# Performance work log

Measured on AMD Instinct MI355X. Metric: run time of the kernel, lower is better.

Reference implementation:

```python
import jax, jax.numpy as jnp
import numpy as np

B, T, F, D = 4, 512, 512, 256


def setup_inputs() -> dict:
    key = jax.random.key(0)
    ks = jax.random.split(key, 7)
    x = jax.random.normal(ks[0], (B, T, F), jnp.float32)
    state = jnp.zeros((B, D, D), jnp.float32)
    init = lambda k, shape, fan: jax.random.normal(k, shape, jnp.float32) / np.sqrt(fan).astype(np.float32)
    Wk = init(ks[1], (F, D), F)
    Wq = init(ks[2], (F, D), F)
    Wv = init(ks[3], (F, D), F)
    Wbeta = init(ks[4], (F, 1), F)
    gamma = jnp.ones((F,), jnp.float32)
    beta_ln = jnp.zeros((F,), jnp.float32)
    Wsc = init(ks[5], (F, D), F)
    bsc = jnp.zeros((D,), jnp.float32)
    return dict(x=x, state=state, Wk=Wk, Wq=Wq, Wv=Wv, Wbeta=Wbeta,
                gamma=gamma, beta_ln=beta_ln, Wsc=Wsc, bsc=bsc)


def _layernorm(x, gamma, beta):
    mu = x.mean(-1, keepdims=True)
    var = x.var(-1, keepdims=True)  # ddof=0, matches torch LayerNorm
    return (x - mu) * jax.lax.rsqrt(var + 1e-5) * gamma + beta


def reference(x, state, Wk, Wq, Wv, Wbeta, gamma, beta_ln, Wsc, bsc):
    xn = _layernorm(x, gamma, beta_ln)                       # [B,T,F]
    K = jax.nn.relu(xn @ Wk)                                 # [B,T,D]
    Q = jax.nn.relu(xn @ Wq)                                 # [B,T,D]
    V = xn @ Wv                                              # [B,T,D]
    beta = jax.nn.sigmoid(xn @ Wbeta)                        # [B,T,1]
    # sum normalization
    K = K / (1e-5 + K.sum(-1, keepdims=True))
    Q = Q / (1e-5 + Q.sum(-1, keepdims=True))

    def step(s, inp):
        k, v, b = inp                                        # k,v:[B,D], b:[B,1]
        vbar = jnp.einsum('bij,bj->bi', s, k)                # retrieve
        s = s + (b * (v - vbar))[:, :, None] * k[:, None, :] # outer-product write
        return s, s

    Kt = jnp.moveaxis(K, 1, 0)  # [T,B,D]
    Vt = jnp.moveaxis(V, 1, 0)
    bt = jnp.moveaxis(beta, 1, 0)  # [T,B,1]
    _, states = jax.lax.scan(step, state, (Kt, Vt, bt))      # [T,B,D,D]
    states = jnp.moveaxis(states, 0, 1)                      # [B,T,D,D]

    y = jnp.einsum('btij,btj->bti', states, Q)               # [B,T,D]
    y = y + xn @ Wsc + bsc                                   # residual shortcut
    return y, states
```

## Files before the change

### kernel.cpp

```cpp
#include <hip/hip_runtime.h>
#include <math.h>

#define Bc 4
#define Tc 512
#define Fc 512
#define Dc 256
#define RPB 8
#define PF 4
#define CH 16
#define RS 2

typedef float floatx4 __attribute__((ext_vector_type(4)));

__device__ __forceinline__ float wred(float v) {
#pragma unroll
  for (int off = 32; off; off >>= 1) v += __shfl_xor(v, off, 64);
  return v;
}

__device__ __forceinline__ void wred2_dpp(float& a, float& c) {
#define DPP_STEP(ctrl, rmask)                                                 \
  {                                                                           \
    float ta = __int_as_float(__builtin_amdgcn_update_dpp(                    \
        0, __float_as_int(a), (ctrl), (rmask), 0xf, true));                   \
    float tc = __int_as_float(__builtin_amdgcn_update_dpp(                    \
        0, __float_as_int(c), (ctrl), (rmask), 0xf, true));                   \
    a += ta;                                                                  \
    c += tc;                                                                  \
  }
  DPP_STEP(0x111, 0xf)
  DPP_STEP(0x112, 0xf)
  DPP_STEP(0x114, 0xf)
  DPP_STEP(0x118, 0xf)
  DPP_STEP(0x142, 0xa)
  DPP_STEP(0x143, 0xc)
#undef DPP_STEP
  a = __int_as_float(__builtin_amdgcn_readlane(__float_as_int(a), 63));
  c = __int_as_float(__builtin_amdgcn_readlane(__float_as_int(c), 63));
}

__global__ __launch_bounds__(256) void proj_kernel(
    const float* __restrict__ x, const float* __restrict__ Wk,
    const float* __restrict__ Wq, const float* __restrict__ Wv,
    const float* __restrict__ Wb, const float* __restrict__ gamma,
    const float* __restrict__ beta_ln, const float* __restrict__ Wsc,
    const float* __restrict__ bsc, float* __restrict__ Ko,
    float* __restrict__ Qo, float* __restrict__ Vo, float* __restrict__ ysco,
    float* __restrict__ betao, float* __restrict__ kqo) {
  __shared__ __align__(16) float xn[RPB][Fc];
  __shared__ float red[4][32];
  __shared__ float fin[32];

  const int tid = threadIdx.x;
  const int wave = tid >> 6, lane = tid & 63;
  const int row0 = blockIdx.x * RPB;

#pragma unroll
  for (int rr = 0; rr < 2; ++rr) {
    const int r = wave * 2 + rr;
    const float* xr = x + (size_t)(row0 + r) * Fc;
    float4 a = *(const float4*)&xr[lane * 8];
    float4 b = *(const float4*)&xr[lane * 8 + 4];
    float s8 = a.x + a.y + a.z + a.w + b.x + b.y + b.z + b.w;
    float mu = wred(s8) * (1.0f / Fc);
    float d0 = a.x - mu, d1 = a.y - mu, d2 = a.z - mu, d3 = a.w - mu;
    float d4 = b.x - mu, d5 = b.y - mu, d6 = b.z - mu, d7 = b.w - mu;
    float sq = d0 * d0 + d1 * d1 + d2 * d2 + d3 * d3 + d4 * d4 + d5 * d5 +
               d6 * d6 + d7 * d7;
    float var = wred(sq) * (1.0f / Fc);
    float rs = rsqrtf(var + 1e-5f);
    float4 g0 = *(const float4*)&gamma[lane * 8];
    float4 g1 = *(const float4*)&gamma[lane * 8 + 4];
    float4 bl0 = *(const float4*)&beta_ln[lane * 8];
    float4 bl1 = *(const float4*)&beta_ln[lane * 8 + 4];
    float4 o0 = make_float4(d0 * rs * g0.x + bl0.x, d1 * rs * g0.y + bl0.y,
                            d2 * rs * g0.z + bl0.z, d3 * rs * g0.w + bl0.w);
    float4 o1 = make_float4(d4 * rs * g1.x + bl1.x, d5 * rs * g1.y + bl1.y,
                            d6 * rs * g1.z + bl1.z, d7 * rs * g1.w + bl1.w);
    *(float4*)&xn[r][lane * 8] = o0;
    *(float4*)&xn[r][lane * 8 + 4] = o1;
  }
  __syncthreads();

  const int d = tid;
  float accK[RPB], accQ[RPB], accV[RPB], accS[RPB];
#pragma unroll
  for (int r = 0; r < RPB; ++r) accK[r] = accQ[r] = accV[r] = accS[r] = 0.0f;

  for (int f = 0; f < Fc; f += 4) {
    float wk[4], wq[4], wv[4], ws[4];
#pragma unroll
    for (int ff = 0; ff < 4; ++ff) {
      wk[ff] = Wk[(size_t)(f + ff) * Dc + d];
      wq[ff] = Wq[(size_t)(f + ff) * Dc + d];
      wv[ff] = Wv[(size_t)(f + ff) * Dc + d];
      ws[ff] = Wsc[(size_t)(f + ff) * Dc + d];
    }
#pragma unroll
    for (int r = 0; r < RPB; ++r) {
      float4 xr = *(const float4*)&xn[r][f];
      accK[r] = fmaf(xr.w, wk[3], fmaf(xr.z, wk[2], fmaf(xr.y, wk[1], fmaf(xr.x, wk[0], accK[r]))));
      accQ[r] = fmaf(xr.w, wq[3], fmaf(xr.z, wq[2], fmaf(xr.y, wq[1], fmaf(xr.x, wq[0], accQ[r]))));
      accV[r] = fmaf(xr.w, wv[3], fmaf(xr.z, wv[2], fmaf(xr.y, wv[1], fmaf(xr.x, wv[0], accV[r]))));
      accS[r] = fmaf(xr.w, ws[3], fmaf(xr.z, ws[2], fmaf(xr.y, ws[1], fmaf(xr.x, ws[0], accS[r]))));
    }
  }

  float pk[RPB], pq[RPB];
#pragma unroll
  for (int r = 0; r < RPB; ++r) {
    pk[r] = fmaxf(accK[r], 0.0f);
    pq[r] = fmaxf(accQ[r], 0.0f);
  }
#pragma unroll
  for (int r = 0; r < RPB; ++r) {
    float p0 = wred(pk[r]);
    float p1 = wred(pq[r]);
    float p2 = wred(pk[r] * pq[r]);
    float pb = xn[r][tid] * Wb[tid] + xn[r][tid + 256] * Wb[tid + 256];
    float p3 = wred(pb);
    if (lane == 0) {
      red[wave][r * 4 + 0] = p0;
      red[wave][r * 4 + 1] = p1;
      red[wave][r * 4 + 2] = p2;
      red[wave][r * 4 + 3] = p3;
    }
  }
  __syncthreads();
  if (tid < 32) fin[tid] = red[0][tid] + red[1][tid] + red[2][tid] + red[3][tid];
  __syncthreads();

#pragma unroll
  for (int r = 0; r < RPB; ++r) {
    size_t row = (size_t)(row0 + r);
    float invK = 1.0f / (1e-5f + fin[r * 4 + 0]);
    float invQ = 1.0f / (1e-5f + fin[r * 4 + 1]);
    Ko[row * Dc + d] = pk[r] * invK;
    Qo[row * Dc + d] = pq[r] * invQ;
    Vo[row * Dc + d] = accV[r];
    ysco[row * Dc + d] = accS[r] + bsc[d];
  }
  if (tid < RPB) {
    size_t row = (size_t)(row0 + tid);
    float invK = 1.0f / (1e-5f + fin[tid * 4 + 0]);
    float invQ = 1.0f / (1e-5f + fin[tid * 4 + 1]);
    betao[row] = 1.0f / (1.0f + expf(-fin[tid * 4 + 3]));
    kqo[row] = fin[tid * 4 + 2] * invK * invQ;
  }
}

__global__ __launch_bounds__(512) void scan_kernel(
    const float* __restrict__ S0, const float* __restrict__ K,
    const float* __restrict__ Q, const float* __restrict__ V,
    const float* __restrict__ ysc, const float* __restrict__ beta,
    const float* __restrict__ kq, float* __restrict__ yout,
    float* __restrict__ states) {
  __shared__ __align__(16) float ring_k[RS][CH][Dc];
  __shared__ float ring_u[RS][CH][4];
  __shared__ int prog_a[4];
  __shared__ int prog_b[4];

  const int tid = threadIdx.x;
  const int wave = tid >> 6, lane = tid & 63;
  const int bid = blockIdx.x;
  const int xcd = bid & 7;
  const int slot = bid >> 3;
  const int b = xcd >> 1;
  const int sub = ((xcd & 1) << 5) | slot;
  const int i0 = sub * 4;

  if (tid < 4) {
    prog_a[tid] = 0;
    prog_b[tid] = 0;
  }
  __syncthreads();

  if (wave < 4) {
    const int i = i0 + wave;
    float4 s = *(const float4*)&S0[((size_t)(b * Dc + i)) * Dc + lane * 4];

    const float* Kb = K + (size_t)b * Tc * Dc;
    const float* Qb = Q + (size_t)b * Tc * Dc;
    const float* Vb = V + (size_t)b * Tc * Dc;
    const float* Yb = ysc + (size_t)b * Tc * Dc;
    const float* bb_p = beta + (size_t)b * Tc;
    const float* kq_p = kq + (size_t)b * Tc;

    float4 kb[PF], qb[PF];
    float vb[PF], ybv[PF], bbv[PF], kqb[PF];
#pragma unroll
    for (int j = 0; j < PF; ++j) {
      kb[j] = *(const float4*)&Kb[(size_t)j * Dc + lane * 4];
      qb[j] = *(const float4*)&Qb[(size_t)j * Dc + lane * 4];
      vb[j] = Vb[(size_t)j * Dc + i];
      ybv[j] = Yb[(size_t)j * Dc + i];
      bbv[j] = bb_p[j];
      kqb[j] = kq_p[j];
    }

    for (int c = 0; c < Tc / CH; ++c) {
      if (c >= RS) {
        const int need = c - RS + 1;
#pragma unroll
        for (int m = 0; m < 4; ++m) {
          while (__hip_atomic_load(&prog_b[m], __ATOMIC_ACQUIRE,
                                   __HIP_MEMORY_SCOPE_WORKGROUP) < need)
            __builtin_amdgcn_s_sleep(2);
        }
      }
      const int r = c & (RS - 1);
      const int tb = c * CH;

      for (int t0 = tb; t0 < tb + CH; t0 += PF) {
#pragma unroll
        for (int p = 0; p < PF; ++p) {
          const int t = t0 + p;
          const float4 k = kb[p];
          const float4 q = qb[p];
          const float vv = vb[p];
          const float yb = ybv[p];
          const float bbs = bbv[p];
          const float kqv = kqb[p];

          const int tn = (t + PF < Tc) ? t + PF : Tc - 1;
          kb[p] = *(const float4*)&Kb[(size_t)tn * Dc + lane * 4];
          qb[p] = *(const float4*)&Qb[(size_t)tn * Dc + lane * 4];
          vb[p] = Vb[(size_t)tn * Dc + i];
          ybv[p] = Yb[(size_t)tn * Dc + i];
          bbv[p] = bb_p[tn];
          kqb[p] = kq_p[tn];

          float a = (s.x * k.x + s.y * k.y) + (s.z * k.z + s.w * k.w);
          float c2 = (s.x * q.x + s.y * q.y) + (s.z * q.z + s.w * q.w);
          wred2_dpp(a, c2);

          const float wcoef = bbs * (vv - a);
          s.x = fmaf(wcoef, k.x, s.x);
          s.y = fmaf(wcoef, k.y, s.y);
          s.z = fmaf(wcoef, k.z, s.z);
          s.w = fmaf(wcoef, k.w, s.w);

          const int j = t - tb;
          if (wave == 0) *(float4*)&ring_k[r][j][lane * 4] = k;
          if (lane == 0) {
            ring_u[r][j][wave] = wcoef;
            yout[((size_t)b * Tc + t) * Dc + i] = c2 + wcoef * kqv + yb;
          }
        }
      }
      __threadfence_block();
      __hip_atomic_store(&prog_a[wave], c + 1, __ATOMIC_RELEASE,
                         __HIP_MEMORY_SCOPE_WORKGROUP);
    }
  } else {
    const int wv = wave - 4;
    const int i = i0 + wv;
    float4 s = *(const float4*)&S0[((size_t)(b * Dc + i)) * Dc + lane * 4];

    for (int c = 0; c < Tc / CH; ++c) {
      const int need = c + 1;
      while (__hip_atomic_load(&prog_a[wv], __ATOMIC_ACQUIRE,
                               __HIP_MEMORY_SCOPE_WORKGROUP) < need)
        __builtin_amdgcn_s_sleep(2);
      while (__hip_atomic_load(&prog_a[0], __ATOMIC_ACQUIRE,
                               __HIP_MEMORY_SCOPE_WORKGROUP) < need)
        __builtin_amdgcn_s_sleep(2);

      const int r = c & (RS - 1);
      const int tb = c * CH;
#pragma unroll
      for (int j = 0; j < CH; ++j) {
        const float u = ring_u[r][j][wv];
        const float4 k = *(const float4*)&ring_k[r][j][lane * 4];
        s.x = fmaf(u, k.x, s.x);
        s.y = fmaf(u, k.y, s.y);
        s.z = fmaf(u, k.z, s.z);
        s.w = fmaf(u, k.w, s.w);
        floatx4 sv;
        sv.x = s.x; sv.y = s.y; sv.z = s.z; sv.w = s.w;
        __builtin_nontemporal_store(
            sv, (floatx4*)&states[(((size_t)b * Tc + tb + j) * Dc + i) * Dc +
                                  lane * 4]);
      }
      __threadfence_block();
      __hip_atomic_store(&prog_b[wv], c + 1, __ATOMIC_RELEASE,
                         __HIP_MEMORY_SCOPE_WORKGROUP);
    }
  }
}

extern "C" void kernel_launch(void* const* d_in, const int* in_sizes, int n_in,
                              void* d_out, int out_size, void* d_ws,
                              size_t ws_size, hipStream_t stream) {
  const float* x = (const float*)d_in[0];
  const float* S0 = (const float*)d_in[1];
  const float* Wk = (const float*)d_in[2];
  const float* Wq = (const float*)d_in[3];
  const float* Wv = (const float*)d_in[4];
  const float* Wb = (const float*)d_in[5];
  const float* gamma = (const float*)d_in[6];
  const float* beta_ln = (const float*)d_in[7];
  const float* Wsc = (const float*)d_in[8];
  const float* bsc = (const float*)d_in[9];

  float* out = (float*)d_out;
  float* yout = out;
  float* states = out + (size_t)Bc * Tc * Dc;

  const size_t BTD = (size_t)Bc * Tc * Dc;
  float* ws = (float*)d_ws;
  float* K = ws;
  float* Q = K + BTD;
  float* V = Q + BTD;
  float* ysc = V + BTD;
  float* beta = ysc + BTD;
  float* kq = beta + (size_t)Bc * Tc;

  proj_kernel<<<(Bc * Tc) / RPB, 256, 0, stream>>>(
      x, Wk, Wq, Wv, Wb, gamma, beta_ln, Wsc, bsc, K, Q, V, ysc, beta, kq);
  scan_kernel<<<(Bc * Dc) / 4, 512, 0, stream>>>(S0, K, Q, V, ysc, beta, kq,
                                                 yout, states);
}
```

Baseline: 173.4 us.

## Offload y stores to writer waves, batch per-chunk scalars via readlane, deepen ring

The recurrence waves now load the per-chunk V, shortcut, beta and kq scalars once per 16-step chunk, one per lane, and prefetch the next chunk's set. Each step extracts its values with readlane. The y output is computed but written to LDS alongside the write coefficient, and the state-writer waves store it to global memory. The k-row copy into LDS is spread across the four recurrence waves, so writer waves now wait on all four of them. The ring buffer depth grows from 2 to 4, which lets the serial recurrence run further ahead of the state-writing waves at the cost of more LDS.

Result: faster. 155.7 us (-10.2%).

```diff
diff --git a/kernel.cpp b/kernel.cpp
--- a/kernel.cpp
+++ b/kernel.cpp
@@ -8,7 +8,8 @@
 #define RPB 8
 #define PF 4
 #define CH 16
-#define RS 2
+#define RS 4
+#define NC (Tc / CH)
 
 typedef float floatx4 __attribute__((ext_vector_type(4)));
 
@@ -16,6 +17,10 @@
 #pragma unroll
   for (int off = 32; off; off >>= 1) v += __shfl_xor(v, off, 64);
   return v;
+}
+
+__device__ __forceinline__ float rl(float v, int l) {
+  return __int_as_float(__builtin_amdgcn_readlane(__float_as_int(v), l));
 }
 
 __device__ __forceinline__ void wred2_dpp(float& a, float& c) {
@@ -35,8 +40,8 @@
   DPP_STEP(0x142, 0xa)
   DPP_STEP(0x143, 0xc)
 #undef DPP_STEP
-  a = __int_as_float(__builtin_amdgcn_readlane(__float_as_int(a), 63));
-  c = __int_as_float(__builtin_amdgcn_readlane(__float_as_int(c), 63));
+  a = rl(a, 63);
+  c = rl(c, 63);
 }
 
 __global__ __launch_bounds__(256) void proj_kernel(
@@ -156,7 +161,7 @@
     const float* __restrict__ kq, float* __restrict__ yout,
     float* __restrict__ states) {
   __shared__ __align__(16) float ring_k[RS][CH][Dc];
-  __shared__ float ring_u[RS][CH][4];
+  __shared__ float2 ring_uy[RS][CH][4];
   __shared__ int prog_a[4];
   __shared__ int prog_b[4];
 
@@ -187,18 +192,18 @@
     const float* kq_p = kq + (size_t)b * Tc;
 
     float4 kb[PF], qb[PF];
-    float vb[PF], ybv[PF], bbv[PF], kqb[PF];
 #pragma unroll
     for (int j = 0; j < PF; ++j) {
       kb[j] = *(const float4*)&Kb[(size_t)j * Dc + lane * 4];
       qb[j] = *(const float4*)&Qb[(size_t)j * Dc + lane * 4];
-      vb[j] = Vb[(size_t)j * Dc + i];
-      ybv[j] = Yb[(size_t)j * Dc + i];
-      bbv[j] = bb_p[j];
-      kqb[j] = kq_p[j];
-    }
-
-    for (int c = 0; c < Tc / CH; ++c) {
+    }
+    const int sl = lane & 15;
+    float vcur = Vb[(size_t)sl * Dc + i];
+    float ycur = Yb[(size_t)sl * Dc + i];
+    float bcur = bb_p[sl];
+    float kqcur = kq_p[sl];
+
+    for (int c = 0; c < NC; ++c) {
       if (c >= RS) {
         const int need = c - RS + 1;
 #pragma unroll
@@ -208,79 +213,85 @@
             __builtin_amdgcn_s_sleep(2);
         }
       }
+      const int cn = (c + 1 < NC) ? c + 1 : c;
+      const int tbn = cn * CH;
+      float vnxt = Vb[(size_t)(tbn + sl) * Dc + i];
+      float ynxt = Yb[(size_t)(tbn + sl) * Dc + i];
+      float bnxt = bb_p[tbn + sl];
+      float kqnxt = kq_p[tbn + sl];
+
       const int r = c & (RS - 1);
       const int tb = c * CH;
-
-      for (int t0 = tb; t0 < tb + CH; t0 += PF) {
-#pragma unroll
-        for (int p = 0; p < PF; ++p) {
-          const int t = t0 + p;
-          const float4 k = kb[p];
-          const float4 q = qb[p];
-          const float vv = vb[p];
-          const float yb = ybv[p];
-          const float bbs = bbv[p];
-          const float kqv = kqb[p];
-
-          const int tn = (t + PF < Tc) ? t + PF : Tc - 1;
-          kb[p] = *(const float4*)&Kb[(size_t)tn * Dc + lane * 4];
-          qb[p] = *(const float4*)&Qb[(size_t)tn * Dc + lane * 4];
-          vb[p] = Vb[(size_t)tn * Dc + i];
-          ybv[p] = Yb[(size_t)tn * Dc + i];
-          bbv[p] = bb_p[tn];
-          kqb[p] = kq_p[tn];
-
-          float a = (s.x * k.x + s.y * k.y) + (s.z * k.z + s.w * k.w);
-          float c2 = (s.x * q.x + s.y * q.y) + (s.z * q.z + s.w * q.w);
-          wred2_dpp(a, c2);
-
-          const float wcoef = bbs * (vv - a);
-          s.x = fmaf(wcoef, k.x, s.x);
-          s.y = fmaf(wcoef, k.y, s.y);
-          s.z = fmaf(wcoef, k.z, s.z);
-          s.w = fmaf(wcoef, k.w, s.w);
-
-          const int j = t - tb;
-          if (wave == 0) *(float4*)&ring_k[r][j][lane * 4] = k;
-          if (lane == 0) {
-            ring_u[r][j][wave] = wcoef;
-            yout[((size_t)b * Tc + t) * Dc + i] = c2 + wcoef * kqv + yb;
-          }
+#pragma unroll
+      for (int j = 0; j < CH; ++j) {
+        const int t = tb + j;
+        const float4 k = kb[j & (PF - 1)];
+        const float4 q = qb[j & (PF - 1)];
+        const float vv = rl(vcur, j);
+        const float yb = rl(ycur, j);
+        const float bbs = rl(bcur, j);
+        const float kqv = rl(kqcur, j);
+
+        const int tn = (t + PF < Tc) ? t + PF : Tc - 1;
+        kb[j & (PF - 1)] = *(const float4*)&Kb[(size_t)tn * Dc + lane * 4];
+        qb[j & (PF - 1)] = *(const float4*)&Qb[(size_t)tn * Dc + lane * 4];
+
+        float a = (s.x * k.x + s.y * k.y) + (s.z * k.z + s.w * k.w);
+        float c2 = (s.x * q.x + s.y * q.y) + (s.z * q.z + s.w * q.w);
+        wred2_dpp(a, c2);
+
+        const float wcoef = bbs * (vv - a);
+        s.x = fmaf(wcoef, k.x, s.x);
+        s.y = fmaf(wcoef, k.y, s.y);
+        s.z = fmaf(wcoef, k.z, s.z);
+        s.w = fmaf(wcoef, k.w, s.w);
+
+        if (wave == (j & 3)) *(float4*)&ring_k[r][j][lane * 4] = k;
+        if (lane == 0) {
+          float2 uy;
+          uy.x = wcoef;
+          uy.y = c2 + wcoef * kqv + yb;
+          ring_uy[r][j][wave] = uy;
         }
       }
       __threadfence_block();
       __hip_atomic_store(&prog_a[wave], c + 1, __ATOMIC_RELEASE,
                          __HIP_MEMORY_SCOPE_WORKGROUP);
+      vcur = vnxt;
+      ycur = ynxt;
+      bcur = bnxt;
+      kqcur = kqnxt;
     }
   } else {
     const int wv = wave - 4;
     const int i = i0 + wv;
     float4 s = *(const float4*)&S0[((size_t)(b * Dc + i)) * Dc + lane * 4];
 
-    for (int c = 0; c < Tc / CH; ++c) {
+    for (int c = 0; c < NC; ++c) {
       const int need = c + 1;
-      while (__hip_atomic_load(&prog_a[wv], __ATOMIC_ACQUIRE,
-                               __HIP_MEMORY_SCOPE_WORKGROUP) < need)
-        __builtin_amdgcn_s_sleep(2);
-      while (__hip_atomic_load(&prog_a[0], __ATOMIC_ACQUIRE,
-                               __HIP_MEMORY_SCOPE_WORKGROUP) < need)
-        __builtin_amdgcn_s_sleep(2);
+#pragma unroll
+      for (int m = 0; m < 4; ++m) {
+        while (__hip_atomic_load(&prog_a[m], __ATOMIC_ACQUIRE,
+                                 __HIP_MEMORY_SCOPE_WORKGROUP) < need)
+          __builtin_amdgcn_s_sleep(2);
+      }
 
       const int r = c & (RS - 1);
       const int tb = c * CH;
 #pragma unroll
       for (int j = 0; j < CH; ++j) {
-        const float u = ring_u[r][j][wv];
+        const float2 uy = ring_uy[r][j][wv];
         const float4 k = *(const float4*)&ring_k[r][j][lane * 4];
-        s.x = fmaf(u, k.x, s.x);
-        s.y = fmaf(u, k.y, s.y);
-        s.z = fmaf(u, k.z, s.z);
-        s.w = fmaf(u, k.w, s.w);
+        s.x = fmaf(uy.x, k.x, s.x);
+        s.y = fmaf(uy.x, k.y, s.y);
+        s.z = fmaf(uy.x, k.z, s.z);
+        s.w = fmaf(uy.x, k.w, s.w);
         floatx4 sv;
         sv.x = s.x; sv.y = s.y; sv.z = s.z; sv.w = s.w;
         __builtin_nontemporal_store(
             sv, (floatx4*)&states[(((size_t)b * Tc + tb + j) * Dc + i) * Dc +
                                   lane * 4]);
+        if (lane == 0) yout[((size_t)b * Tc + tb + j) * Dc + i] = uy.y;
       }
       __threadfence_block();
       __hip_atomic_store(&prog_b[wv], c + 1, __ATOMIC_RELEASE,
```
